# Performance work log

Measured on AMD Instinct MI355X. Metric: run time of the kernel, lower is better.

## Reference

```python
import jax, jax.numpy as jnp
import numpy as np

NUM_BOXES = 512
NUM_COORDS = 200000
C = 128
MAX_SELECTED = 262144  # static pad size for the ragged output
P_INSIDE = 0.002       # expected ~204.8k selected rows < MAX_SELECTED


def setup_inputs() -> dict:
    key = jax.random.key(0)
    k1, k2, k3 = jax.random.split(key, 3)
    coords = jax.random.randint(k1, (NUM_COORDS, 4), 0, 256, dtype=jnp.int32)
    features = jax.random.normal(k2, (NUM_COORDS, C), dtype=jnp.float32)
    is_inside = jax.random.uniform(k3, (NUM_BOXES, NUM_COORDS)) < P_INSIDE
    return {"coords": coords, "features": features, "is_inside": is_inside,
            "max_selected": MAX_SELECTED}


def reference(coords, features, is_inside, max_selected):
    # Faithful to select_coords/select_features, but WITHOUT materializing the
    # dense (num_boxes, num_coords, C) expand: compute flat nonzero indices of
    # the mask directly and gather once. Output is padded to a static size
    # (padded rows zeroed) since jax requires static shapes.
    num_boxes, num_coords = is_inside.shape
    total = num_boxes * num_coords
    flat_idx = jnp.nonzero(is_inside.ravel(), size=max_selected, fill_value=total)[0]
    valid = flat_idx < total                      # [K] pad mask
    safe = jnp.where(valid, flat_idx, 0)
    box_idx = (safe // num_coords).astype(jnp.int32)   # [K]
    coord_idx = safe % num_coords                       # [K]
    # select_features: features[None].expand(...)[is_inside]
    selected_features = jnp.where(valid[:, None], features[coord_idx], 0.0)  # [K, C]
    # select_coords: cat(coords[:, :-1] gathered, box index)
    sel_xyz = coords[coord_idx, :-1]                    # [K, 3]
    ext_coords = jnp.concatenate([sel_xyz, box_idx[:, None]], axis=-1)  # [K, 4]
    extended_coordinates = jnp.where(valid[:, None], ext_coords, 0)
    return extended_coordinates, selected_features
```

## Files before the change

### kernel.cpp

```cpp
#include <hip/hip_runtime.h>


#define BS   256
#define WPT  8
#define WPB  (BS*WPT)
#define FLAG_AGG (1ull<<62)
#define FLAG_PRE (2ull<<62)

__global__ void __launch_bounds__(BS) compact_lookback(
    const uint4* __restrict__ d, long long totalElems, int wordsTotal,
    int numTiles, int max_sel,
    unsigned long long* __restrict__ state,
    int* __restrict__ ticketPtr,
    int* __restrict__ selIdx, int* __restrict__ totalOut)
{
  __shared__ int sh_ticket;
  __shared__ int sh_excl;
  __shared__ int wsum[BS/64];
  const int tid  = threadIdx.x;
  const int lane = tid & 63;
  const int wid  = tid >> 6;

  if (tid == 0) sh_ticket = atomicAdd(ticketPtr, 1);
  __syncthreads();
  const int t     = sh_ticket;
  const int wBase = t * WPB;

  unsigned m[WPT];
  int cnt = 0;
  #pragma unroll
  for (int k = 0; k < WPT; ++k){
    const int w = wBase + k*BS + tid;
    unsigned mm = 0;
    if (w < wordsTotal){
      const long long e0 = (long long)w << 5;
      if (e0 + 31 < totalElems){
        const uint4* base = d + 8*(long long)w;
        #pragma unroll
        for (int q = 0; q < 8; ++q){
          uint4 x = base[q];
          mm |= ((unsigned)(x.x!=0) << (4*q))   | ((unsigned)(x.y!=0) << (4*q+1)) |
                ((unsigned)(x.z!=0) << (4*q+2)) | ((unsigned)(x.w!=0) << (4*q+3));
        }
      } else {
        const unsigned* p32 = (const unsigned*)d;
        for (int b2 = 0; b2 < 32 && e0 + b2 < totalElems; ++b2)
          if (p32[e0 + b2]) mm |= (1u << b2);
      }
    }
    m[k] = mm;
    cnt += __popc(mm);
  }

  int red = cnt;
  for (int off = 32; off > 0; off >>= 1) red += __shfl_down(red, off, 64);
  if (lane == 0) wsum[wid] = red;
  __syncthreads();
  const int agg = wsum[0] + wsum[1] + wsum[2] + wsum[3];

  if (tid == 0){
    unsigned long long p = (t == 0 ? FLAG_PRE : FLAG_AGG) | (unsigned long long)(unsigned)agg;
    __hip_atomic_store(&state[t], p, __ATOMIC_RELAXED, __HIP_MEMORY_SCOPE_AGENT);
    if (t == 0){
      sh_excl = 0;
      if (numTiles == 1) *totalOut = agg;
    }
  }
  if (t > 0 && wid == 0){
    int run = 0;
    int j = t - 1;
    while (true){
      const int idx = j - lane;
      unsigned long long s;
      if (idx >= 0){
        s = __hip_atomic_load(&state[idx], __ATOMIC_RELAXED, __HIP_MEMORY_SCOPE_AGENT);
        while (s == 0ull){
          __builtin_amdgcn_s_sleep(2);
          s = __hip_atomic_load(&state[idx], __ATOMIC_RELAXED, __HIP_MEMORY_SCOPE_AGENT);
        }
      } else {
        s = FLAG_PRE;
      }
      const unsigned long long ball = __ballot((s >> 62) == 2ull);
      const int val = (int)(s & 0xFFFFFFFFull);
      int contrib;
      int stop = 0;
      if (ball){
        const int firstPre = __ffsll((long long)ball) - 1;
        contrib = (lane <= firstPre) ? val : 0;
        stop = 1;
      } else {
        contrib = val;
      }
      for (int off = 32; off > 0; off >>= 1) contrib += __shfl_down(contrib, off, 64);
      if (lane == 0) run += contrib;
      if (stop) break;
      j -= 64;
    }
    if (lane == 0){
      sh_excl = run;
      __hip_atomic_store(&state[t],
                         FLAG_PRE | (unsigned long long)(unsigned)(run + agg),
                         __ATOMIC_RELAXED, __HIP_MEMORY_SCOPE_AGENT);
      if (t == numTiles - 1) *totalOut = run + agg;
    }
  }
  __syncthreads();

  int running = sh_excl;
  #pragma unroll
  for (int k = 0; k < WPT; ++k){
    unsigned mm = m[k];
    const int c = __popc(mm);
    int incl = c;
    for (int off = 1; off < 64; off <<= 1){
      int tv = __shfl_up(incl, off, 64);
      if (lane >= off) incl += tv;
    }
    if (lane == 63) wsum[wid] = incl;
    __syncthreads();
    int wbase = 0;
    for (int ww = 0; ww < wid; ++ww) wbase += wsum[ww];
    int iterTotal = 0;
    for (int ww = 0; ww < BS/64; ++ww) iterTotal += wsum[ww];
    int pos = running + wbase + incl - c;
    if (mm){
      const int w = wBase + k*BS + tid;
      const long long e0 = (long long)w << 5;
      while (mm){
        const int b = __ffs(mm) - 1;
        mm &= mm - 1;
        if (pos < max_sel) selIdx[pos] = (int)(e0 + b);
        ++pos;
      }
    }
    running += iterTotal;
    __syncthreads();
  }
}

__global__ void __launch_bounds__(BS) gather_kernel(
    const int* __restrict__ selIdx, const int* __restrict__ totalPtr,
    const int4* __restrict__ coords, const float4* __restrict__ feat,
    int num_coords, int c4, int max_sel,
    float4* __restrict__ outExt, float4* __restrict__ outFeat)
{
  const int lane    = threadIdx.x & 31;
  const int g0      = (blockIdx.x*blockDim.x + threadIdx.x) >> 5;
  const int gstride = (gridDim.x*blockDim.x) >> 5;
  int total = *totalPtr;
  if (total > max_sel) total = max_sel;
  const float4 z = make_float4(0.f, 0.f, 0.f, 0.f);
  for (int r = g0; r < max_sel; r += gstride){
    float4* dst = outFeat + (long long)r*c4;
    if (r < total){
      const int flat = selIdx[r];
      const unsigned box = (unsigned)flat / (unsigned)num_coords;
      const int ci = flat - (int)box*num_coords;
      const float4* src = feat + (long long)ci*c4;
      for (int c = lane; c < c4; c += 32) dst[c] = src[c];
      if (lane == 0){
        int4 cc = coords[ci];
        outExt[r] = make_float4((float)cc.x, (float)cc.y, (float)cc.z, (float)box);
      }
    } else {
      for (int c = lane; c < c4; c += 32) dst[c] = z;
      if (lane == 0) outExt[r] = z;
    }
  }
}

extern "C" void kernel_launch(void* const* d_in, const int* in_sizes, int n_in,
                              void* d_out, int out_size, void* d_ws, size_t ws_size,
                              hipStream_t stream){
  const int*   coords   = (const int*)d_in[0];
  const float* features = (const float*)d_in[1];
  const void*  inside   = d_in[2];

  const int num_coords = in_sizes[0] / 4;
  const int C          = in_sizes[1] / num_coords;
  const int c4         = C / 4;
  const long long totalElems = (long long)in_sizes[2];
  const int max_sel    = out_size / (4 + C);

  const int wordsTotal = (int)((totalElems + 31) / 32);
  const int numTiles   = (wordsTotal + WPB - 1) / WPB;

  unsigned long long* state = (unsigned long long*)d_ws;
  int* ticket = (int*)(state + numTiles);
  int* total  = ticket + 1;
  int* selIdx = ticket + 2;

  hipMemsetAsync(state, 0, (size_t)numTiles*8 + 8, stream);

  hipLaunchKernelGGL(compact_lookback, dim3(numTiles), dim3(BS), 0, stream,
                     (const uint4*)inside, totalElems, wordsTotal, numTiles, max_sel,
                     state, ticket, selIdx, total);

  hipLaunchKernelGGL(gather_kernel, dim3(2048), dim3(BS), 0, stream,
                     selIdx, total, (const int4*)coords, (const float4*)features,
                     num_coords, c4, max_sel,
                     (float4*)d_out,
                     (float4*)((float*)d_out + (long long)max_sel*4));
}
```

Baseline: 681.1 us.

## Replace decoupled look-back compaction with two-pass count and emit kernels

The single-pass stream compaction with ticketed decoupled look-back is split into a pass that packs the 4-byte bool mask into bitwords and writes per-tile counts, and an emit pass that computes each tile's base by summing all preceding tile counts and then scatters indices. This removes the serial inter-block spin-waiting and the memset of the state array. In exchange it adds an extra launch, writes and re-reads a packed mask buffer, and makes each emit block sum up to numTiles counts, which grows quadratically with tile count.

```diff
diff --git a/kernel.cpp b/kernel.cpp
--- a/kernel.cpp
+++ b/kernel.cpp
@@ -1,121 +1,83 @@
 #include <hip/hip_runtime.h>
 
 
-#define BS   256
-#define WPT  8
-#define WPB  (BS*WPT)
-#define FLAG_AGG (1ull<<62)
-#define FLAG_PRE (2ull<<62)
+#define BS  256
+#define WPT 8
+#define WPB (BS*WPT)
 
-__global__ void __launch_bounds__(BS) compact_lookback(
+__global__ void __launch_bounds__(BS) pack_count(
     const uint4* __restrict__ d, long long totalElems, int wordsTotal,
-    int numTiles, int max_sel,
-    unsigned long long* __restrict__ state,
-    int* __restrict__ ticketPtr,
-    int* __restrict__ selIdx, int* __restrict__ totalOut)
+    unsigned* __restrict__ maskOut, int* __restrict__ counts)
 {
-  __shared__ int sh_ticket;
-  __shared__ int sh_excl;
-  __shared__ int wsum[BS/64];
-  const int tid  = threadIdx.x;
-  const int lane = tid & 63;
-  const int wid  = tid >> 6;
-
-  if (tid == 0) sh_ticket = atomicAdd(ticketPtr, 1);
-  __syncthreads();
-  const int t     = sh_ticket;
-  const int wBase = t * WPB;
-
-  unsigned m[WPT];
+  const int tid = threadIdx.x;
+  const int wBase = blockIdx.x * WPB;
   int cnt = 0;
   #pragma unroll
   for (int k = 0; k < WPT; ++k){
     const int w = wBase + k*BS + tid;
-    unsigned mm = 0;
-    if (w < wordsTotal){
-      const long long e0 = (long long)w << 5;
-      if (e0 + 31 < totalElems){
-        const uint4* base = d + 8*(long long)w;
-        #pragma unroll
-        for (int q = 0; q < 8; ++q){
-          uint4 x = base[q];
-          mm |= ((unsigned)(x.x!=0) << (4*q))   | ((unsigned)(x.y!=0) << (4*q+1)) |
-                ((unsigned)(x.z!=0) << (4*q+2)) | ((unsigned)(x.w!=0) << (4*q+3));
-        }
-      } else {
-        const unsigned* p32 = (const unsigned*)d;
-        for (int b2 = 0; b2 < 32 && e0 + b2 < totalElems; ++b2)
-          if (p32[e0 + b2]) mm |= (1u << b2);
+    if (w >= wordsTotal) break;
+    const long long e0 = (long long)w << 5;
+    unsigned m = 0;
+    if (e0 + 31 < totalElems){
+      const uint4* base = d + 8*(long long)w;
+      #pragma unroll
+      for (int q = 0; q < 8; ++q){
+        uint4 x = base[q];
+        m |= ((unsigned)(x.x!=0) << (4*q))   | ((unsigned)(x.y!=0) << (4*q+1)) |
+             ((unsigned)(x.z!=0) << (4*q+2)) | ((unsigned)(x.w!=0) << (4*q+3));
       }
+    } else {
+      const unsigned* p32 = (const unsigned*)d;
+      for (int b2 = 0; b2 < 32 && e0 + b2 < totalElems; ++b2)
+        if (p32[e0 + b2]) m |= (1u << b2);
     }
-    m[k] = mm;
-    cnt += __popc(mm);
+    maskOut[w] = m;
+    cnt += __popc(m);
   }
+  const int lane = tid & 63, wid = tid >> 6;
+  for (int off = 32; off > 0; off >>= 1) cnt += __shfl_down(cnt, off, 64);
+  __shared__ int wsum[BS/64];
+  if (lane == 0) wsum[wid] = cnt;
+  __syncthreads();
+  if (tid == 0)
+    counts[blockIdx.x] = wsum[0] + wsum[1] + wsum[2] + wsum[3];
+}
 
-  int red = cnt;
+__global__ void __launch_bounds__(BS) emit_kernel(
+    const unsigned* __restrict__ mask, const int* __restrict__ counts,
+    int wordsTotal, int numTiles, int max_sel,
+    int* __restrict__ outIdx, int* __restrict__ totalOut)
+{
+  const int tid = threadIdx.x;
+  const int lane = tid & 63, wid = tid >> 6;
+  const int bid = blockIdx.x;
+  __shared__ int wsum[BS/64];
+  __shared__ int sh_base;
+
+  int pre = 0;
+  for (int i = tid; i < bid; i += BS) pre += counts[i];
+  int red = pre;
   for (int off = 32; off > 0; off >>= 1) red += __shfl_down(red, off, 64);
   if (lane == 0) wsum[wid] = red;
   __syncthreads();
-  const int agg = wsum[0] + wsum[1] + wsum[2] + wsum[3];
-
   if (tid == 0){
-    unsigned long long p = (t == 0 ? FLAG_PRE : FLAG_AGG) | (unsigned long long)(unsigned)agg;
-    __hip_atomic_store(&state[t], p, __ATOMIC_RELAXED, __HIP_MEMORY_SCOPE_AGENT);
-    if (t == 0){
-      sh_excl = 0;
-      if (numTiles == 1) *totalOut = agg;
-    }
-  }
-  if (t > 0 && wid == 0){
-    int run = 0;
-    int j = t - 1;
-    while (true){
-      const int idx = j - lane;
-      unsigned long long s;
-      if (idx >= 0){
-        s = __hip_atomic_load(&state[idx], __ATOMIC_RELAXED, __HIP_MEMORY_SCOPE_AGENT);
-        while (s == 0ull){
-          __builtin_amdgcn_s_sleep(2);
-          s = __hip_atomic_load(&state[idx], __ATOMIC_RELAXED, __HIP_MEMORY_SCOPE_AGENT);
-        }
-      } else {
-        s = FLAG_PRE;
-      }
-      const unsigned long long ball = __ballot((s >> 62) == 2ull);
-      const int val = (int)(s & 0xFFFFFFFFull);
-      int contrib;
-      int stop = 0;
-      if (ball){
-        const int firstPre = __ffsll((long long)ball) - 1;
-        contrib = (lane <= firstPre) ? val : 0;
-        stop = 1;
-      } else {
-        contrib = val;
-      }
-      for (int off = 32; off > 0; off >>= 1) contrib += __shfl_down(contrib, off, 64);
-      if (lane == 0) run += contrib;
-      if (stop) break;
-      j -= 64;
-    }
-    if (lane == 0){
-      sh_excl = run;
-      __hip_atomic_store(&state[t],
-                         FLAG_PRE | (unsigned long long)(unsigned)(run + agg),
-                         __ATOMIC_RELAXED, __HIP_MEMORY_SCOPE_AGENT);
-      if (t == numTiles - 1) *totalOut = run + agg;
-    }
+    const int base = wsum[0] + wsum[1] + wsum[2] + wsum[3];
+    sh_base = base;
+    if (bid == numTiles - 1) *totalOut = base + counts[bid];
   }
   __syncthreads();
 
-  int running = sh_excl;
+  int running = sh_base;
+  const int wBase = bid * WPB;
   #pragma unroll
-  for (int k = 0; k < WPT; ++k){
-    unsigned mm = m[k];
-    const int c = __popc(mm);
-    int incl = c;
+  for (int it = 0; it < WPT; ++it){
+    const int w = wBase + it*BS + tid;
+    unsigned m = (w < wordsTotal) ? mask[w] : 0u;
+    const int cnt = __popc(m);
+    int incl = cnt;
     for (int off = 1; off < 64; off <<= 1){
-      int tv = __shfl_up(incl, off, 64);
-      if (lane >= off) incl += tv;
+      int t = __shfl_up(incl, off, 64);
+      if (lane >= off) incl += t;
     }
     if (lane == 63) wsum[wid] = incl;
     __syncthreads();
@@ -123,14 +85,14 @@
     for (int ww = 0; ww < wid; ++ww) wbase += wsum[ww];
     int iterTotal = 0;
     for (int ww = 0; ww < BS/64; ++ww) iterTotal += wsum[ww];
-    int pos = running + wbase + incl - c;
-    if (mm){
-      const int w = wBase + k*BS + tid;
+    int pos = running + wbase + incl - cnt;
+    if (m){
       const long long e0 = (long long)w << 5;
+      unsigned mm = m;
       while (mm){
         const int b = __ffs(mm) - 1;
         mm &= mm - 1;
-        if (pos < max_sel) selIdx[pos] = (int)(e0 + b);
+        if (pos < max_sel) outIdx[pos] = (int)(e0 + b);
         ++pos;
       }
     }
@@ -186,16 +148,16 @@
   const int wordsTotal = (int)((totalElems + 31) / 32);
   const int numTiles   = (wordsTotal + WPB - 1) / WPB;
 
-  unsigned long long* state = (unsigned long long*)d_ws;
-  int* ticket = (int*)(state + numTiles);
-  int* total  = ticket + 1;
-  int* selIdx = ticket + 2;
+  int* counts  = (int*)d_ws;
+  int* total   = counts + numTiles;
+  int* selIdx  = total + 1;
+  unsigned* maskBuf = (unsigned*)(selIdx + max_sel);
 
-  hipMemsetAsync(state, 0, (size_t)numTiles*8 + 8, stream);
+  hipLaunchKernelGGL(pack_count, dim3(numTiles), dim3(BS), 0, stream,
+                     (const uint4*)inside, totalElems, wordsTotal, maskBuf, counts);
 
-  hipLaunchKernelGGL(compact_lookback, dim3(numTiles), dim3(BS), 0, stream,
-                     (const uint4*)inside, totalElems, wordsTotal, numTiles, max_sel,
-                     state, ticket, selIdx, total);
+  hipLaunchKernelGGL(emit_kernel, dim3(numTiles), dim3(BS), 0, stream,
+                     maskBuf, counts, wordsTotal, numTiles, max_sel, selIdx, total);
 
   hipLaunchKernelGGL(gather_kernel, dim3(2048), dim3(BS), 0, stream,
                      selIdx, total, (const int4*)coords, (const float4*)features,
```

Measured after the change: 662.7 us. 2.7% less time.
